# Performance work log

Measured on AMD Instinct MI355X. Metric: run time of the kernel, lower is better.

Reference implementation:

```python
import jax, jax.numpy as jnp
import numpy as np

B, C, L, N = 128, 3, 256, 4

def setup_inputs() -> dict:
    key = jax.random.key(0)
    kx, kX, kY, kW, kH = jax.random.split(key, 5)
    x = jax.random.normal(kx, (B, C, L, L), dtype=jnp.float32)
    X = jax.random.randint(kX, (N, B), 0, L, dtype=jnp.int32)
    Y = jax.random.randint(kY, (N, B), 0, L, dtype=jnp.int32)
    W = jax.random.randint(kW, (N, B), 0, 64, dtype=jnp.int32)
    H = jax.random.randint(kH, (N, B), 0, 64, dtype=jnp.int32)
    return {"x": x, "X": X, "Y": Y, "W": W, "H": H}

def reference(x, X, Y, W, H):
    # x: [B, C, L, L]; X/Y/W/H: [N, B] int32 box bounds per cutout per sample.
    length = x.shape[2]
    idx = jnp.arange(length, dtype=jnp.int32)  # [L]
    # mask_x: [N, B, L] -> columns inside [X, X+W]
    mask_x = (idx[None, None, :] >= X[:, :, None]) & (idx[None, None, :] <= (X + W)[:, :, None])
    # mask_y: [N, B, L] -> rows inside [Y, Y+H]
    mask_y = (idx[None, None, :] >= Y[:, :, None]) & (idx[None, None, :] <= (Y + H)[:, :, None])
    # 'square' shape: pixel masked if inside any of the N boxes.
    # Fused outer product per box, any over N: [B, L, L]
    mask = jnp.any(mask_y[:, :, :, None] & mask_x[:, :, None, :], axis=0)
    # broadcast over channels; zero masked pixels
    return jnp.where(mask[:, None, :, :], jnp.zeros((), dtype=x.dtype), x)
```

## Files before the change

### kernel.cpp

```cpp
#include <hip/hip_runtime.h>


constexpr int BB = 128;
constexpr int CC = 3;
constexpr int LL = 256;
constexpr int NN = 4;

__global__ __launch_bounds__(256) void mask_square_kernel(
    const float4* __restrict__ x,
    const int* __restrict__ Xb,
    const int* __restrict__ Yb,
    const int* __restrict__ Wb,
    const int* __restrict__ Hb,
    float4* __restrict__ out)
{
    const int i4   = blockIdx.x * 256 + threadIdx.x;
    const int col0 = (i4 & 63) << 2;
    const int row  = (i4 >> 6) & (LL - 1);
    const int bc   = i4 >> 14;
    const int b    = bc / CC;

    float4 v = x[i4];

    int m0 = 0, m1 = 0, m2 = 0, m3 = 0;
#pragma unroll
    for (int n = 0; n < NN; ++n) {
        const int Xn = Xb[n * BB + b];
        const int Yn = Yb[n * BB + b];
        const int Wn = Wb[n * BB + b];
        const int Hn = Hb[n * BB + b];
        const int rin = (row >= Yn) & (row <= Yn + Hn);
        const int lo = Xn, hi = Xn + Wn;
        m0 |= rin & (col0     >= lo) & (col0     <= hi);
        m1 |= rin & (col0 + 1 >= lo) & (col0 + 1 <= hi);
        m2 |= rin & (col0 + 2 >= lo) & (col0 + 2 <= hi);
        m3 |= rin & (col0 + 3 >= lo) & (col0 + 3 <= hi);
    }
    if (m0) v.x = 0.0f;
    if (m1) v.y = 0.0f;
    if (m2) v.z = 0.0f;
    if (m3) v.w = 0.0f;

    out[i4] = v;
}

extern "C" void kernel_launch(void* const* d_in, const int* in_sizes, int n_in,
                              void* d_out, int out_size, void* d_ws, size_t ws_size,
                              hipStream_t stream) {
    const float4* x  = (const float4*)d_in[0];
    const int*    Xb = (const int*)d_in[1];
    const int*    Yb = (const int*)d_in[2];
    const int*    Wb = (const int*)d_in[3];
    const int*    Hb = (const int*)d_in[4];
    float4*       o  = (float4*)d_out;

    const int total4 = BB * CC * LL * LL / 4;
    const int blocks = total4 / 256;
    mask_square_kernel<<<blocks, 256, 0, stream>>>(x, Xb, Yb, Wb, Hb, o);
}
```

Baseline: 178.3 us.

## Process eight float4s per thread with nontemporal loads/stores and hoisted column mask

Each thread now handles eight rows of float4 data instead of one. All eight loads are issued up front and use nontemporal load/store builtins. The per-box column mask is computed once as a 4-bit pattern and reused across the rows, and the range checks are replaced by single unsigned comparisons. This is meant to add memory-level parallelism, cut per-element index and mask work, and reduce box-bound loads. The cost is eight times fewer blocks and higher register use per thread.

```diff
diff --git a/kernel.cpp b/kernel.cpp
--- a/kernel.cpp
+++ b/kernel.cpp
@@ -5,56 +5,94 @@
 constexpr int CC = 3;
 constexpr int LL = 256;
 constexpr int NN = 4;
+constexpr int U  = 8;
+
+typedef float f32x4 __attribute__((ext_vector_type(4)));
 
 __global__ __launch_bounds__(256) void mask_square_kernel(
-    const float4* __restrict__ x,
+    const f32x4* __restrict__ x,
     const int* __restrict__ Xb,
     const int* __restrict__ Yb,
     const int* __restrict__ Wb,
     const int* __restrict__ Hb,
-    float4* __restrict__ out)
+    f32x4* __restrict__ out)
 {
-    const int i4   = blockIdx.x * 256 + threadIdx.x;
-    const int col0 = (i4 & 63) << 2;
-    const int row  = (i4 >> 6) & (LL - 1);
-    const int bc   = i4 >> 14;
+    const int blk  = blockIdx.x;
+    const int bc   = blk >> 3;
     const int b    = bc / CC;
+    const int row0 = (blk & 7) << 5;
+    const int tid  = threadIdx.x;
+    const int base = blk * 2048 + tid;
 
-    float4 v = x[i4];
+    const int col0 = (tid & 63) << 2;
+    const int r0   = row0 + (tid >> 6);
 
-    int m0 = 0, m1 = 0, m2 = 0, m3 = 0;
+    f32x4 v0 = __builtin_nontemporal_load(&x[base + 256 * 0]);
+    f32x4 v1 = __builtin_nontemporal_load(&x[base + 256 * 1]);
+    f32x4 v2 = __builtin_nontemporal_load(&x[base + 256 * 2]);
+    f32x4 v3 = __builtin_nontemporal_load(&x[base + 256 * 3]);
+    f32x4 v4 = __builtin_nontemporal_load(&x[base + 256 * 4]);
+    f32x4 v5 = __builtin_nontemporal_load(&x[base + 256 * 5]);
+    f32x4 v6 = __builtin_nontemporal_load(&x[base + 256 * 6]);
+    f32x4 v7 = __builtin_nontemporal_load(&x[base + 256 * 7]);
+
+    int m[U];
+#pragma unroll
+    for (int u = 0; u < U; ++u) m[u] = 0;
+
 #pragma unroll
     for (int n = 0; n < NN; ++n) {
         const int Xn = Xb[n * BB + b];
         const int Yn = Yb[n * BB + b];
         const int Wn = Wb[n * BB + b];
         const int Hn = Hb[n * BB + b];
-        const int rin = (row >= Yn) & (row <= Yn + Hn);
-        const int lo = Xn, hi = Xn + Wn;
-        m0 |= rin & (col0     >= lo) & (col0     <= hi);
-        m1 |= rin & (col0 + 1 >= lo) & (col0 + 1 <= hi);
-        m2 |= rin & (col0 + 2 >= lo) & (col0 + 2 <= hi);
-        m3 |= rin & (col0 + 3 >= lo) & (col0 + 3 <= hi);
+
+        const int dc = col0 - Xn;
+        const int colbits =
+            ((unsigned)(dc    ) <= (unsigned)Wn ? 1 : 0) |
+            ((unsigned)(dc + 1) <= (unsigned)Wn ? 2 : 0) |
+            ((unsigned)(dc + 2) <= (unsigned)Wn ? 4 : 0) |
+            ((unsigned)(dc + 3) <= (unsigned)Wn ? 8 : 0);
+
+#pragma unroll
+        for (int u = 0; u < U; ++u) {
+            const int rin = (unsigned)(r0 + 4 * u - Yn) <= (unsigned)Hn;
+            m[u] |= rin ? colbits : 0;
+        }
     }
-    if (m0) v.x = 0.0f;
-    if (m1) v.y = 0.0f;
-    if (m2) v.z = 0.0f;
-    if (m3) v.w = 0.0f;
 
-    out[i4] = v;
+#define APPLY_STORE(u, vv)                                          \
+    {                                                               \
+        f32x4 w = vv;                                               \
+        if (m[u] & 1) w.x = 0.0f;                                   \
+        if (m[u] & 2) w.y = 0.0f;                                   \
+        if (m[u] & 4) w.z = 0.0f;                                   \
+        if (m[u] & 8) w.w = 0.0f;                                   \
+        __builtin_nontemporal_store(w, &out[base + 256 * (u)]);     \
+    }
+
+    APPLY_STORE(0, v0)
+    APPLY_STORE(1, v1)
+    APPLY_STORE(2, v2)
+    APPLY_STORE(3, v3)
+    APPLY_STORE(4, v4)
+    APPLY_STORE(5, v5)
+    APPLY_STORE(6, v6)
+    APPLY_STORE(7, v7)
+#undef APPLY_STORE
 }
 
 extern "C" void kernel_launch(void* const* d_in, const int* in_sizes, int n_in,
                               void* d_out, int out_size, void* d_ws, size_t ws_size,
                               hipStream_t stream) {
-    const float4* x  = (const float4*)d_in[0];
-    const int*    Xb = (const int*)d_in[1];
-    const int*    Yb = (const int*)d_in[2];
-    const int*    Wb = (const int*)d_in[3];
-    const int*    Hb = (const int*)d_in[4];
-    float4*       o  = (float4*)d_out;
+    const f32x4* x  = (const f32x4*)d_in[0];
+    const int*   Xb = (const int*)d_in[1];
+    const int*   Yb = (const int*)d_in[2];
+    const int*   Wb = (const int*)d_in[3];
+    const int*   Hb = (const int*)d_in[4];
+    f32x4*       o  = (f32x4*)d_out;
 
     const int total4 = BB * CC * LL * LL / 4;
-    const int blocks = total4 / 256;
+    const int blocks = total4 / (256 * U);
     mask_square_kernel<<<blocks, 256, 0, stream>>>(x, Xb, Yb, Wb, Hb, o);
 }
```

After: 172.8 us. -3.1%, faster.
